# Optimization experiments

Measured on AMD Instinct MI355X. Metric: run time of the kernel, lower is better.

## Reference

```python
import math
import jax, jax.numpy as jnp
import numpy as np

NEG = -1e10


def _rope_cos_sin(T, head_dim, dtype):
    # theta_i = 10000^(-2*(i-1)/dim), i=1..dim/2  ->  j=0..dim/2-1: 10000^(-2j/dim)
    j = jnp.arange(head_dim // 2, dtype=jnp.float32)
    inv_freq = 1.0 / (10000.0 ** (2.0 * j / head_dim))
    t = jnp.arange(T, dtype=jnp.float32)
    ang = t[:, None] * inv_freq[None, :]          # [T, hd/2]
    return jnp.cos(ang).astype(dtype), jnp.sin(ang).astype(dtype)


def _apply_rope(x, cos, sin):
    # x: [B, H, T, hd]; complex multiply (cos + i sin) * (x0 + i x1)
    B, H, T, hd = x.shape
    xr = x.reshape(B, H, T, hd // 2, 2)
    x0, x1 = xr[..., 0], xr[..., 1]
    c = cos[None, None]  # [1,1,T,hd/2]
    s = sin[None, None]
    o0 = c * x0 - s * x1
    o1 = s * x0 + c * x1
    return jnp.stack([o0, o1], axis=-1).reshape(B, H, T, hd)


def setup_inputs() -> dict:
    key = jax.random.key(0)
    ks = jax.random.split(key, 9)
    B, T, C = 2, 2048, 1024
    std = 0.02
    return {
        "x": jax.random.normal(ks[0], (B, T, C), jnp.float32),
        "Wq": jax.random.normal(ks[1], (C, C), jnp.float32) * std,
        "bq": jnp.zeros((C,), jnp.float32),
        "Wk": jax.random.normal(ks[2], (C, C), jnp.float32) * std,
        "bk": jnp.zeros((C,), jnp.float32),
        "Wv": jax.random.normal(ks[3], (C, C), jnp.float32) * std,
        "bv": jnp.zeros((C,), jnp.float32),
        "Wp": jax.random.normal(ks[4], (C, C), jnp.float32) * std,
        "bp": jnp.zeros((C,), jnp.float32),
    }


def reference(x, Wq, bq, Wk, bk, Wv, bv, Wp, bp):
    B, T, C = x.shape
    H = 16
    hd = C // H

    def heads(y):  # [B,T,C] -> [B,H,T,hd]
        return y.reshape(B, T, H, hd).transpose(0, 2, 1, 3)

    q = heads(x @ Wq.T + bq)
    k = heads(x @ Wk.T + bk)
    v = heads(x @ Wv.T + bv)

    cos, sin = _rope_cos_sin(T, hd, x.dtype)
    q = _apply_rope(q, cos, sin)
    k = _apply_rope(k, cos, sin)

    att = jnp.einsum('bhqd,bhkd->bhqk', q, k) * (1.0 / math.sqrt(hd))
    causal = jnp.tril(jnp.ones((T, T), bool))
    att = jnp.where(causal[None, None], att, jnp.asarray(NEG, att.dtype))
    att = jax.nn.softmax(att, axis=-1)

    y = jnp.einsum('bhqk,bhkd->bhqd', att, v)
    y = y.transpose(0, 2, 1, 3).reshape(B, T, C)
    return y @ Wp.T + bp
```

## Files before the change

kernel.cpp:

```cpp
#include <hip/hip_runtime.h>
#include <math.h>

typedef unsigned short u16;
typedef unsigned int u32;
typedef unsigned long long u64;
typedef __attribute__((ext_vector_type(8))) short short8;
typedef __attribute__((ext_vector_type(4))) float f32x4;
typedef __attribute__((ext_vector_type(4))) u16 u16x4;
typedef __attribute__((ext_vector_type(4))) u32 u32x4;

#define AS1 __attribute__((address_space(1)))
#define AS3 __attribute__((address_space(3)))

#define QSCALE 0.18033688011112042f

__device__ __forceinline__ u16 f2bf(float f) {
  union { float f; u32 i; } u; u.f = f;
  u32 r = u.i + 0x7FFFu + ((u.i >> 16) & 1u);
  return (u16)(r >> 16);
}

__device__ __forceinline__ u32 pk_bf16(float a, float b) {
  u32 r;
  asm volatile("v_cvt_pk_bf16_f32 %0, %1, %2" : "=v"(r) : "v"(a), "v"(b));
  return r;
}

__device__ __forceinline__ void gl_lds16(const void* g, void* l) {
  __builtin_amdgcn_global_load_lds((const AS1 u32*)g, (AS3 u32*)l, 16, 0, 0);
}

#define MFMA32(a, b, c) __builtin_amdgcn_mfma_f32_16x16x32_bf16(a, b, c, 0, 0, 0)

__global__ void cvt_all(const float* __restrict__ x,
                        const float* __restrict__ Wq, const float* __restrict__ Wk,
                        const float* __restrict__ Wv, const float* __restrict__ Wp,
                        u16* __restrict__ xb,
                        u16* __restrict__ Wqb, u16* __restrict__ Wkb,
                        u16* __restrict__ Wvb, u16* __restrict__ Wpb,
                        float* __restrict__ cosT, float* __restrict__ sinT,
                        int n4x, int n4tot) {
  int i = blockIdx.x * 256 + threadIdx.x;
  if (i >= n4tot) {
    int k = i - n4tot;
    int t = k >> 5, j = k & 31;
    float inv = powf(10000.0f, -(float)j / 32.0f);
    float ang = (float)t * inv;
    cosT[k] = cosf(ang);
    sinT[k] = sinf(ang);
    return;
  }
  const float* src; u16* dst; int off;
  if (i < n4x) { src = x; dst = xb; off = i; }
  else {
    int wi = i - n4x;
    int sel = wi >> 18;
    off = wi & ((1 << 18) - 1);
    src = sel == 0 ? Wq : sel == 1 ? Wk : sel == 2 ? Wv : Wp;
    dst = sel == 0 ? Wqb : sel == 1 ? Wkb : sel == 2 ? Wvb : Wpb;
  }
  float4 v = ((const float4*)src)[off];
  u16x4 o = { f2bf(v.x), f2bf(v.y), f2bf(v.z), f2bf(v.w) };
  ((u16x4*)dst)[off] = o;
}

__global__ __launch_bounds__(256, 2) void gemm_qkv(
    const u16* __restrict__ xb,
    const u16* __restrict__ Wqb, const u16* __restrict__ Wkb, const u16* __restrict__ Wvb,
    const float* __restrict__ bq, const float* __restrict__ bk, const float* __restrict__ bv,
    const float* __restrict__ cosT, const float* __restrict__ sinT,
    u16* __restrict__ Qb, u16* __restrict__ Kb, u16* __restrict__ Vb) {
  const int K = 1024, N = 1024;
  __shared__ __attribute__((aligned(16))) u16 As[128 * 32];
  __shared__ __attribute__((aligned(16))) u16 Bs[128 * 32];
  const int tid = threadIdx.x;
  const int lane = tid & 63;
  const int hi = lane >> 4, cc = lane & 15;
  const int w = tid >> 6, wm = w >> 1, wn = w & 1;
  const int sel = blockIdx.x >> 3;
  const int row0 = blockIdx.y * 128, col0 = (blockIdx.x & 7) * 128;
  const u16* W = sel == 0 ? Wqb : sel == 1 ? Wkb : Wvb;
  const float* bias = sel == 0 ? bq : sel == 1 ? bk : bv;
  u16* Out = sel == 0 ? Qb : sel == 1 ? Kb : Vb;

  const int lr = tid >> 2;
  const int lk = (((tid & 3) ^ (lr & 3)) * 8);
  const u16* Ag0 = xb + (size_t)(row0 + lr) * K + lk;
  const u16* Ag1 = xb + (size_t)(row0 + 64 + lr) * K + lk;
  const u16* Wg0 = W + (size_t)(col0 + lr) * K + lk;
  const u16* Wg1 = W + (size_t)(col0 + 64 + lr) * K + lk;
  u16* Al0 = As + tid * 8;
  u16* Al1 = As + 2048 + tid * 8;
  u16* Bl0 = Bs + tid * 8;
  u16* Bl1 = Bs + 2048 + tid * 8;

  const int rb = (hi ^ (cc & 3)) * 8;

  f32x4 acc[4][4];
#pragma unroll
  for (int m = 0; m < 4; ++m)
#pragma unroll
    for (int n = 0; n < 4; ++n) acc[m][n] = f32x4{0.f, 0.f, 0.f, 0.f};

  for (int k0 = 0; k0 < K; k0 += 32) {
    __syncthreads();
    gl_lds16(Ag0 + k0, Al0);
    gl_lds16(Ag1 + k0, Al1);
    gl_lds16(Wg0 + k0, Bl0);
    gl_lds16(Wg1 + k0, Bl1);
    __syncthreads();
    short8 a[4], b[4];
#pragma unroll
    for (int m = 0; m < 4; ++m)
      a[m] = *(const short8*)(As + (wm * 64 + m * 16 + cc) * 32 + rb);
#pragma unroll
    for (int n = 0; n < 4; ++n)
      b[n] = *(const short8*)(Bs + (wn * 64 + n * 16 + cc) * 32 + rb);
#pragma unroll
    for (int m = 0; m < 4; ++m)
#pragma unroll
      for (int n = 0; n < 4; ++n)
        acc[m][n] = MFMA32(a[m], b[n], acc[m][n]);
  }

  if (sel < 2) {
    const float qs = (sel == 0) ? QSCALE : 1.0f;
#pragma unroll
    for (int n = 0; n < 4; ++n) {
      const int col = col0 + wn * 64 + n * 16 + cc;
      const int j = (col & 63) >> 1;
      const float bb = bias[col];
#pragma unroll
      for (int m = 0; m < 4; ++m) {
        const int rw = row0 + wm * 64 + m * 16 + hi * 4;
#pragma unroll
        for (int r = 0; r < 4; ++r) {
          const int row = rw + r;
          const int t = row & 2047;
          float v = acc[m][n][r] + bb;
          float pv = __shfl_xor(v, 1);
          float c = cosT[t * 32 + j], s = sinT[t * 32 + j];
          float oo = (cc & 1) ? (s * pv + c * v) : (c * v - s * pv);
          Out[(size_t)row * N + col] = f2bf(oo * qs);
        }
      }
    }
  } else {
#pragma unroll
    for (int n = 0; n < 4; ++n) {
      const int col = col0 + wn * 64 + n * 16 + cc;
      const float bb = bias[col];
#pragma unroll
      for (int m = 0; m < 4; ++m) {
        const int rw = row0 + wm * 64 + m * 16 + hi * 4;
#pragma unroll
        for (int r = 0; r < 4; ++r)
          Out[(size_t)(rw + r) * N + col] = f2bf(acc[m][n][r] + bb);
      }
    }
  }
}

__global__ __launch_bounds__(256, 2) void flash_mfma(
    const u16* __restrict__ Qb, const u16* __restrict__ Kb,
    const u16* __restrict__ Vb, u16* __restrict__ Yb) {
  const int T = 2048, C = 1024;
  __shared__ __attribute__((aligned(16))) u16 Ks[64 * 64];
  __shared__ __attribute__((aligned(16))) u16 Vt[64 * 64];
  __shared__ __attribute__((aligned(16))) u16 Ps[4][16 * 64];

  const int tid = threadIdx.x;
  const int lane = tid & 63;
  const int hi = lane >> 4, cc = lane & 15;
  const int hi4 = hi * 4;
  const int w = tid >> 6;
  const int qtA = blockIdx.x;
  const int qtB = 31 - qtA;
  const int bh = blockIdx.y;
  const size_t hbase = (size_t)(bh >> 4) * T * C + (size_t)(bh & 15) * 64;
  const int qA0w = qtA * 64 + w * 16;
  const int qB0w = qtB * 64 + w * 16;

  short8 qaA0, qaA1, qaB0, qaB1;
  {
    const u16* qp = Qb + hbase + (size_t)(qA0w + cc) * C + hi * 8;
    qaA0 = *(const short8*)qp;
    qaA1 = *(const short8*)(qp + 32);
    qp = Qb + hbase + (size_t)(qB0w + cc) * C + hi * 8;
    qaB0 = *(const short8*)qp;
    qaB1 = *(const short8*)(qp + 32);
  }

  f32x4 oA[4], oB[4];
#pragma unroll
  for (int nt = 0; nt < 4; ++nt) {
    oA[nt] = f32x4{0.f, 0.f, 0.f, 0.f};
    oB[nt] = f32x4{0.f, 0.f, 0.f, 0.f};
  }
  float mA = -1e30f, lA = 0.f, mB = -1e30f, lB = 0.f;

  const int krow = tid >> 2, kcol = (tid & 3) * 16;
  const int vd0 = (tid & 31) * 2, vkey0 = (tid >> 5) * 8;
  const u16* kgp = Kb + hbase + (size_t)krow * C + kcol;
  const u16* vgp = Vb + hbase + (size_t)vkey0 * C + vd0;

  short8 kr0, kr1;
  u32 vr_[8];

  auto LOADT = [&](int kt) {
    const size_t off = (size_t)(kt * 64) * C;
    kr0 = *(const short8*)(kgp + off);
    kr1 = *(const short8*)(kgp + off + 8);
#pragma unroll
    for (int j = 0; j < 8; ++j)
      vr_[j] = *(const u32*)(vgp + off + (size_t)j * C);
  };

  char* KsB = (char*)Ks;
  char* VtB = (char*)Vt;
  char* PsB = (char*)(Ps[w]);

  auto WRITET = [&]() {
    const int kb = krow * 128 + kcol * 2;
    const int ksw = (krow & 7) << 4;
    *(short8*)(KsB + (kb ^ ksw)) = kr0;
    *(short8*)(KsB + ((kb + 16) ^ ksw)) = kr1;
    u32 lo0 = (vr_[0] & 0xFFFFu) | (vr_[1] << 16);
    u32 lo1 = (vr_[2] & 0xFFFFu) | (vr_[3] << 16);
    u32 lo2 = (vr_[4] & 0xFFFFu) | (vr_[5] << 16);
    u32 lo3 = (vr_[6] & 0xFFFFu) | (vr_[7] << 16);
    u32 hh0 = (vr_[0] >> 16) | (vr_[1] & 0xFFFF0000u);
    u32 hh1 = (vr_[2] >> 16) | (vr_[3] & 0xFFFF0000u);
    u32 hh2 = (vr_[4] >> 16) | (vr_[5] & 0xFFFF0000u);
    u32 hh3 = (vr_[6] >> 16) | (vr_[7] & 0xFFFF0000u);
    const int d1 = vd0 + 1;
    u32x4 vlo = {lo0, lo1, lo2, lo3};
    u32x4 vhi = {hh0, hh1, hh2, hh3};
    *(u32x4*)(VtB + ((vd0 * 128 + vkey0 * 2) ^ ((vd0 & 7) << 4))) = vlo;
    *(u32x4*)(VtB + ((d1 * 128 + vkey0 * 2) ^ ((d1 & 7) << 4))) = vhi;
  };

  const int ksw2 = (cc & 7) << 4;
  short8 kf[4][2];

  auto CHUNK = [&](const short8& qa0, const short8& qa1, f32x4* o,
                   float& mrow, float& lsum, bool diag) {
    f32x4 s[4];
#pragma unroll
    for (int nt = 0; nt < 4; ++nt) {
      f32x4 z = f32x4{0.f, 0.f, 0.f, 0.f};
      z = MFMA32(kf[nt][0], qa0, z);
      z = MFMA32(kf[nt][1], qa1, z);
      s[nt] = z;
    }
    if (diag) {
      const int qloc = w * 16 + cc;
#pragma unroll
      for (int nt = 0; nt < 4; ++nt)
#pragma unroll
        for (int r = 0; r < 4; ++r)
          if (nt * 16 + hi4 + r > qloc) s[nt][r] = -1e30f;
    }
    float tm = s[0][0];
#pragma unroll
    for (int nt = 0; nt < 4; ++nt)
#pragma unroll
      for (int r = 0; r < 4; ++r) tm = fmaxf(tm, s[nt][r]);
    tm = fmaxf(tm, __shfl_xor(tm, 16));
    tm = fmaxf(tm, __shfl_xor(tm, 32));

    const bool need = tm > mrow + 8.0f;
    float corr = 1.0f;
    if (need) { corr = exp2f(mrow - tm); mrow = tm; }

    float psum = 0.f;
#pragma unroll
    for (int nt = 0; nt < 4; ++nt) {
      float e0 = exp2f(s[nt][0] - mrow);
      float e1 = exp2f(s[nt][1] - mrow);
      float e2 = exp2f(s[nt][2] - mrow);
      float e3 = exp2f(s[nt][3] - mrow);
      psum += (e0 + e1) + (e2 + e3);
      u32 pr[2] = { pk_bf16(e0, e1), pk_bf16(e2, e3) };
      *(u64*)(PsB + ((cc * 128 + nt * 32 + hi * 8) ^ ksw2)) = *(const u64*)pr;
    }
    psum += __shfl_xor(psum, 16);
    psum += __shfl_xor(psum, 32);
    lsum = lsum * corr + psum;
    if (__any(need)) {
#pragma unroll
      for (int nt = 0; nt < 4; ++nt) o[nt] *= corr;
    }

#pragma unroll
    for (int kc = 0; kc < 2; ++kc) {
      short8 pa = *(const short8*)(PsB + ((cc * 128 + kc * 64 + hi * 16) ^ ksw2));
#pragma unroll
      for (int nt = 0; nt < 4; ++nt) {
        short8 vb = *(const short8*)(VtB + (((nt * 16 + cc) * 128 + kc * 64 + hi * 16) ^ ksw2));
        o[nt] = MFMA32(vb, pa, o[nt]);
      }
    }
  };

  LOADT(0);
  WRITET();
  LOADT(1);
  __syncthreads();

  for (int kt = 0; kt <= qtB; ++kt) {
#pragma unroll
    for (int nt = 0; nt < 4; ++nt) {
      const int kb = (nt * 16 + cc) * 128 + hi * 16;
      kf[nt][0] = *(const short8*)(KsB + (kb ^ ksw2));
      kf[nt][1] = *(const short8*)(KsB + ((kb + 64) ^ ksw2));
    }

    CHUNK(qaB0, qaB1, oB, mB, lB, kt == qtB);
    if (kt <= qtA) CHUNK(qaA0, qaA1, oA, mA, lA, kt == qtA);

    if (kt < qtB) {
      __syncthreads();
      WRITET();
      if (kt + 1 < qtB) LOADT(kt + 2);
      __syncthreads();
    }
  }

  const float ivA = 1.0f / lA, ivB = 1.0f / lB;
#pragma unroll
  for (int nt = 0; nt < 4; ++nt) {
    u16x4 yA = { f2bf(oA[nt][0] * ivA), f2bf(oA[nt][1] * ivA),
                 f2bf(oA[nt][2] * ivA), f2bf(oA[nt][3] * ivA) };
    *(u16x4*)(Yb + hbase + (size_t)(qA0w + cc) * C + nt * 16 + hi4) = yA;
    u16x4 yB = { f2bf(oB[nt][0] * ivB), f2bf(oB[nt][1] * ivB),
                 f2bf(oB[nt][2] * ivB), f2bf(oB[nt][3] * ivB) };
    *(u16x4*)(Yb + hbase + (size_t)(qB0w + cc) * C + nt * 16 + hi4) = yB;
  }
}

__global__ __launch_bounds__(256, 2) void gemm_proj(
    const u16* __restrict__ A, const u16* __restrict__ W,
    const float* __restrict__ bias, float* __restrict__ Out) {
  const int K = 1024, N = 1024;
  __shared__ __attribute__((aligned(16))) u16 As[128 * 32];
  __shared__ __attribute__((aligned(16))) u16 Bs[64 * 32];
  const int tid = threadIdx.x;
  const int lane = tid & 63;
  const int hi = lane >> 4, cc = lane & 15;
  const int w = tid >> 6, wm = w >> 1, wn = w & 1;
  const int row0 = blockIdx.y * 128, col0 = blockIdx.x * 64;

  const int lr = tid >> 2;
  const int lk = (((tid & 3) ^ (lr & 3)) * 8);
  const u16* Ag0 = A + (size_t)(row0 + lr) * K + lk;
  const u16* Ag1 = A + (size_t)(row0 + 64 + lr) * K + lk;
  const u16* Wg0 = W + (size_t)(col0 + lr) * K + lk;
  u16* Al0 = As + tid * 8;
  u16* Al1 = As + 2048 + tid * 8;
  u16* Bl0 = Bs + tid * 8;

  const int rb = (hi ^ (cc & 3)) * 8;

  f32x4 acc[4][2];
#pragma unroll
  for (int m = 0; m < 4; ++m)
#pragma unroll
    for (int n = 0; n < 2; ++n) acc[m][n] = f32x4{0.f, 0.f, 0.f, 0.f};

  for (int k0 = 0; k0 < K; k0 += 32) {
    __syncthreads();
    gl_lds16(Ag0 + k0, Al0);
    gl_lds16(Ag1 + k0, Al1);
    gl_lds16(Wg0 + k0, Bl0);
    __syncthreads();
    short8 a[4], b[2];
#pragma unroll
    for (int m = 0; m < 4; ++m)
      a[m] = *(const short8*)(As + (wm * 64 + m * 16 + cc) * 32 + rb);
#pragma unroll
    for (int n = 0; n < 2; ++n)
      b[n] = *(const short8*)(Bs + (wn * 32 + n * 16 + cc) * 32 + rb);
#pragma unroll
    for (int m = 0; m < 4; ++m)
#pragma unroll
      for (int n = 0; n < 2; ++n)
        acc[m][n] = MFMA32(a[m], b[n], acc[m][n]);
  }

#pragma unroll
  for (int n = 0; n < 2; ++n) {
    const int col = col0 + wn * 32 + n * 16 + cc;
    const float bb = bias[col];
#pragma unroll
    for (int m = 0; m < 4; ++m) {
      const int rw = row0 + wm * 64 + m * 16 + hi * 4;
#pragma unroll
      for (int r = 0; r < 4; ++r)
        Out[(size_t)(rw + r) * N + col] = acc[m][n][r] + bb;
    }
  }
}

extern "C" void kernel_launch(void* const* d_in, const int* in_sizes, int n_in,
                              void* d_out, int out_size, void* d_ws, size_t ws_size,
                              hipStream_t stream) {
  const float* x  = (const float*)d_in[0];
  const float* Wq = (const float*)d_in[1];
  const float* bq = (const float*)d_in[2];
  const float* Wk = (const float*)d_in[3];
  const float* bk = (const float*)d_in[4];
  const float* Wv = (const float*)d_in[5];
  const float* bv = (const float*)d_in[6];
  const float* Wp = (const float*)d_in[7];
  const float* bp = (const float*)d_in[8];
  float* out = (float*)d_out;

  const int B = 2, T = 2048, C = 1024;
  const int M = B * T;
  const size_t MC = (size_t)M * C;
  const size_t CC = (size_t)C * C;

  char* p = (char*)d_ws;
  u16* xb  = (u16*)p;  p += MC * 2;
  u16* Wqb = (u16*)p;  p += CC * 2;
  u16* Wkb = (u16*)p;  p += CC * 2;
  u16* Wvb = (u16*)p;  p += CC * 2;
  u16* Wpb = (u16*)p;  p += CC * 2;
  u16* Qbb = (u16*)p;  p += MC * 2;
  u16* Kbb = (u16*)p;  p += MC * 2;
  u16* Vbb = (u16*)p;  p += MC * 2;
  float* cosT = (float*)p; p += (size_t)T * 32 * 4;
  float* sinT = (float*)p; p += (size_t)T * 32 * 4;

  const int n4x = (int)(MC / 4);
  const int n4tot = n4x + 4 * (int)(CC / 4);
  const int ntot = n4tot + T * 32;
  cvt_all<<<(ntot + 255) / 256, 256, 0, stream>>>(x, Wq, Wk, Wv, Wp,
                                                  xb, Wqb, Wkb, Wvb, Wpb,
                                                  cosT, sinT, n4x, n4tot);

  dim3 gq(24, M / 128);
  gemm_qkv<<<gq, 256, 0, stream>>>(xb, Wqb, Wkb, Wvb, bq, bk, bv, cosT, sinT, Qbb, Kbb, Vbb);

  dim3 fg(16, B * 16);
  flash_mfma<<<fg, 256, 0, stream>>>(Qbb, Kbb, Vbb, xb);

  dim3 gp(C / 64, M / 128);
  gemm_proj<<<gp, 256, 0, stream>>>(xb, Wpb, bp, out);
}
```

Baseline: 128.1 us.

## Double GEMM K-tile to 64 and interleave two query chunks in flash attention

Both GEMM kernels move from a K-step of 32 to 64, using a wider 8-way XOR swizzle in LDS. This halves the number of barrier pairs per K loop and issues more MFMAs between syncs, at the cost of twice the shared memory per block. The flash attention loop now computes QK^T for both query chunks before either softmax, and gives each chunk its own P buffer. It also loads the V fragments once from LDS and reuses them for both PV products, which cuts redundant LDS reads and exposes more independent MFMA work, but raises register pressure.

Result: faster. 124.2 us (-3.1%).

```diff
diff --git a/kernel.cpp b/kernel.cpp
--- a/kernel.cpp
+++ b/kernel.cpp
@@ -71,8 +71,8 @@
     const float* __restrict__ cosT, const float* __restrict__ sinT,
     u16* __restrict__ Qb, u16* __restrict__ Kb, u16* __restrict__ Vb) {
   const int K = 1024, N = 1024;
-  __shared__ __attribute__((aligned(16))) u16 As[128 * 32];
-  __shared__ __attribute__((aligned(16))) u16 Bs[128 * 32];
+  __shared__ __attribute__((aligned(16))) u16 As[128 * 64];
+  __shared__ __attribute__((aligned(16))) u16 Bs[128 * 64];
   const int tid = threadIdx.x;
   const int lane = tid & 63;
   const int hi = lane >> 4, cc = lane & 15;
@@ -83,18 +83,10 @@
   const float* bias = sel == 0 ? bq : sel == 1 ? bk : bv;
   u16* Out = sel == 0 ? Qb : sel == 1 ? Kb : Vb;
 
-  const int lr = tid >> 2;
-  const int lk = (((tid & 3) ^ (lr & 3)) * 8);
-  const u16* Ag0 = xb + (size_t)(row0 + lr) * K + lk;
-  const u16* Ag1 = xb + (size_t)(row0 + 64 + lr) * K + lk;
-  const u16* Wg0 = W + (size_t)(col0 + lr) * K + lk;
-  const u16* Wg1 = W + (size_t)(col0 + 64 + lr) * K + lk;
-  u16* Al0 = As + tid * 8;
-  u16* Al1 = As + 2048 + tid * 8;
-  u16* Bl0 = Bs + tid * 8;
-  u16* Bl1 = Bs + 2048 + tid * 8;
-
-  const int rb = (hi ^ (cc & 3)) * 8;
+  const int lr = tid >> 3;
+  const int lkb = (((tid & 7) ^ (lr & 7)) * 8);
+  const u16* Ag = xb + (size_t)(row0 + lr) * K + lkb;
+  const u16* Wg = W + (size_t)(col0 + lr) * K + lkb;
 
   f32x4 acc[4][4];
 #pragma unroll
@@ -102,25 +94,33 @@
 #pragma unroll
     for (int n = 0; n < 4; ++n) acc[m][n] = f32x4{0.f, 0.f, 0.f, 0.f};
 
-  for (int k0 = 0; k0 < K; k0 += 32) {
+  for (int k0 = 0; k0 < K; k0 += 64) {
     __syncthreads();
-    gl_lds16(Ag0 + k0, Al0);
-    gl_lds16(Ag1 + k0, Al1);
-    gl_lds16(Wg0 + k0, Bl0);
-    gl_lds16(Wg1 + k0, Bl1);
+#pragma unroll
+    for (int j = 0; j < 4; ++j) {
+      gl_lds16(Ag + (size_t)j * 32 * K + k0, As + j * 2048 + tid * 8);
+      gl_lds16(Wg + (size_t)j * 32 * K + k0, Bs + j * 2048 + tid * 8);
+    }
     __syncthreads();
-    short8 a[4], b[4];
-#pragma unroll
-    for (int m = 0; m < 4; ++m)
-      a[m] = *(const short8*)(As + (wm * 64 + m * 16 + cc) * 32 + rb);
-#pragma unroll
-    for (int n = 0; n < 4; ++n)
-      b[n] = *(const short8*)(Bs + (wn * 64 + n * 16 + cc) * 32 + rb);
-#pragma unroll
-    for (int m = 0; m < 4; ++m)
+    short8 a[2][4], b[2][4];
+#pragma unroll
+    for (int kk = 0; kk < 2; ++kk) {
+#pragma unroll
+      for (int m = 0; m < 4; ++m)
+        a[kk][m] = *(const short8*)(As + (wm * 64 + m * 16 + cc) * 64 +
+                                    (((kk * 4 + hi) ^ (cc & 7)) * 8));
 #pragma unroll
       for (int n = 0; n < 4; ++n)
-        acc[m][n] = MFMA32(a[m], b[n], acc[m][n]);
+        b[kk][n] = *(const short8*)(Bs + (wn * 64 + n * 16 + cc) * 64 +
+                                    (((kk * 4 + hi) ^ (cc & 7)) * 8));
+    }
+#pragma unroll
+    for (int kk = 0; kk < 2; ++kk)
+#pragma unroll
+      for (int m = 0; m < 4; ++m)
+#pragma unroll
+        for (int n = 0; n < 4; ++n)
+          acc[m][n] = MFMA32(a[kk][m], b[kk][n], acc[m][n]);
   }
 
   if (sel < 2) {
@@ -167,7 +167,7 @@
   const int T = 2048, C = 1024;
   __shared__ __attribute__((aligned(16))) u16 Ks[64 * 64];
   __shared__ __attribute__((aligned(16))) u16 Vt[64 * 64];
-  __shared__ __attribute__((aligned(16))) u16 Ps[4][16 * 64];
+  __shared__ __attribute__((aligned(16))) u16 Ps[4][2][16 * 64];
 
   const int tid = threadIdx.x;
   const int lane = tid & 63;
@@ -218,7 +218,8 @@
 
   char* KsB = (char*)Ks;
   char* VtB = (char*)Vt;
-  char* PsB = (char*)(Ps[w]);
+  char* PsA_ = (char*)(Ps[w][0]);
+  char* PsB_ = (char*)(Ps[w][1]);
 
   auto WRITET = [&]() {
     const int kb = krow * 128 + kcol * 2;
@@ -241,11 +242,9 @@
   };
 
   const int ksw2 = (cc & 7) << 4;
-  short8 kf[4][2];
-
-  auto CHUNK = [&](const short8& qa0, const short8& qa1, f32x4* o,
-                   float& mrow, float& lsum, bool diag) {
-    f32x4 s[4];
+
+  auto QKT = [&](short8 (&kf)[4][2], const short8& qa0, const short8& qa1,
+                 f32x4 (&s)[4]) {
 #pragma unroll
     for (int nt = 0; nt < 4; ++nt) {
       f32x4 z = f32x4{0.f, 0.f, 0.f, 0.f};
@@ -253,14 +252,9 @@
       z = MFMA32(kf[nt][1], qa1, z);
       s[nt] = z;
     }
-    if (diag) {
-      const int qloc = w * 16 + cc;
-#pragma unroll
-      for (int nt = 0; nt < 4; ++nt)
-#pragma unroll
-        for (int r = 0; r < 4; ++r)
-          if (nt * 16 + hi4 + r > qloc) s[nt][r] = -1e30f;
-    }
+  };
+
+  auto SM = [&](f32x4 (&s)[4], float& mrow, float& lsum, f32x4* o, char* PsX) {
     float tm = s[0][0];
 #pragma unroll
     for (int nt = 0; nt < 4; ++nt)
@@ -268,11 +262,9 @@
       for (int r = 0; r < 4; ++r) tm = fmaxf(tm, s[nt][r]);
     tm = fmaxf(tm, __shfl_xor(tm, 16));
     tm = fmaxf(tm, __shfl_xor(tm, 32));
-
     const bool need = tm > mrow + 8.0f;
     float corr = 1.0f;
     if (need) { corr = exp2f(mrow - tm); mrow = tm; }
-
     float psum = 0.f;
 #pragma unroll
     for (int nt = 0; nt < 4; ++nt) {
@@ -282,7 +274,7 @@
       float e3 = exp2f(s[nt][3] - mrow);
       psum += (e0 + e1) + (e2 + e3);
       u32 pr[2] = { pk_bf16(e0, e1), pk_bf16(e2, e3) };
-      *(u64*)(PsB + ((cc * 128 + nt * 32 + hi * 8) ^ ksw2)) = *(const u64*)pr;
+      *(u64*)(PsX + ((cc * 128 + nt * 32 + hi * 8) ^ ksw2)) = *(const u64*)pr;
     }
     psum += __shfl_xor(psum, 16);
     psum += __shfl_xor(psum, 32);
@@ -291,16 +283,15 @@
 #pragma unroll
       for (int nt = 0; nt < 4; ++nt) o[nt] *= corr;
     }
-
-#pragma unroll
-    for (int kc = 0; kc < 2; ++kc) {
-      short8 pa = *(const short8*)(PsB + ((cc * 128 + kc * 64 + hi * 16) ^ ksw2));
-#pragma unroll
-      for (int nt = 0; nt < 4; ++nt) {
-        short8 vb = *(const short8*)(VtB + (((nt * 16 + cc) * 128 + kc * 64 + hi * 16) ^ ksw2));
-        o[nt] = MFMA32(vb, pa, o[nt]);
-      }
-    }
+  };
+
+  auto MASK = [&](f32x4 (&s)[4]) {
+    const int qloc = w * 16 + cc;
+#pragma unroll
+    for (int nt = 0; nt < 4; ++nt)
+#pragma unroll
+      for (int r = 0; r < 4; ++r)
+        if (nt * 16 + hi4 + r > qloc) s[nt][r] = -1e30f;
   };
 
   LOADT(0);
@@ -309,6 +300,7 @@
   __syncthreads();
 
   for (int kt = 0; kt <= qtB; ++kt) {
+    short8 kf[4][2];
 #pragma unroll
     for (int nt = 0; nt < 4; ++nt) {
       const int kb = (nt * 16 + cc) * 128 + hi * 16;
@@ -316,8 +308,39 @@
       kf[nt][1] = *(const short8*)(KsB + ((kb + 64) ^ ksw2));
     }
 
-    CHUNK(qaB0, qaB1, oB, mB, lB, kt == qtB);
-    if (kt <= qtA) CHUNK(qaA0, qaA1, oA, mA, lA, kt == qtA);
+    const bool actA = (kt <= qtA);
+    f32x4 sB[4], sA[4];
+    QKT(kf, qaB0, qaB1, sB);
+    if (actA) QKT(kf, qaA0, qaA1, sA);
+    if (kt == qtB) MASK(sB);
+    if (actA && kt == qtA) MASK(sA);
+
+    SM(sB, mB, lB, oB, PsB_);
+    if (actA) SM(sA, mA, lA, oA, PsA_);
+
+    short8 vf[2][4];
+#pragma unroll
+    for (int kc = 0; kc < 2; ++kc)
+#pragma unroll
+      for (int nt = 0; nt < 4; ++nt)
+        vf[kc][nt] = *(const short8*)(VtB + (((nt * 16 + cc) * 128 + kc * 64 + hi * 16) ^ ksw2));
+
+#pragma unroll
+    for (int kc = 0; kc < 2; ++kc) {
+      short8 pa = *(const short8*)(PsB_ + ((cc * 128 + kc * 64 + hi * 16) ^ ksw2));
+#pragma unroll
+      for (int nt = 0; nt < 4; ++nt)
+        oB[nt] = MFMA32(vf[kc][nt], pa, oB[nt]);
+    }
+    if (actA) {
+#pragma unroll
+      for (int kc = 0; kc < 2; ++kc) {
+        short8 pa = *(const short8*)(PsA_ + ((cc * 128 + kc * 64 + hi * 16) ^ ksw2));
+#pragma unroll
+        for (int nt = 0; nt < 4; ++nt)
+          oA[nt] = MFMA32(vf[kc][nt], pa, oA[nt]);
+      }
+    }
 
     if (kt < qtB) {
       __syncthreads();
@@ -343,24 +366,18 @@
     const u16* __restrict__ A, const u16* __restrict__ W,
     const float* __restrict__ bias, float* __restrict__ Out) {
   const int K = 1024, N = 1024;
-  __shared__ __attribute__((aligned(16))) u16 As[128 * 32];
-  __shared__ __attribute__((aligned(16))) u16 Bs[64 * 32];
+  __shared__ __attribute__((aligned(16))) u16 As[128 * 64];
+  __shared__ __attribute__((aligned(16))) u16 Bs[64 * 64];
   const int tid = threadIdx.x;
   const int lane = tid & 63;
   const int hi = lane >> 4, cc = lane & 15;
   const int w = tid >> 6, wm = w >> 1, wn = w & 1;
   const int row0 = blockIdx.y * 128, col0 = blockIdx.x * 64;
 
-  const int lr = tid >> 2;
-  const int lk = (((tid & 3) ^ (lr & 3)) * 8);
-  const u16* Ag0 = A + (size_t)(row0 + lr) * K + lk;
-  const u16* Ag1 = A + (size_t)(row0 + 64 + lr) * K + lk;
-  const u16* Wg0 = W + (size_t)(col0 + lr) * K + lk;
-  u16* Al0 = As + tid * 8;
-  u16* Al1 = As + 2048 + tid * 8;
-  u16* Bl0 = Bs + tid * 8;
-
-  const int rb = (hi ^ (cc & 3)) * 8;
+  const int lr = tid >> 3;
+  const int lkb = (((tid & 7) ^ (lr & 7)) * 8);
+  const u16* Ag = A + (size_t)(row0 + lr) * K + lkb;
+  const u16* Wg = W + (size_t)(col0 + lr) * K + lkb;
 
   f32x4 acc[4][2];
 #pragma unroll
@@ -368,24 +385,34 @@
 #pragma unroll
     for (int n = 0; n < 2; ++n) acc[m][n] = f32x4{0.f, 0.f, 0.f, 0.f};
 
-  for (int k0 = 0; k0 < K; k0 += 32) {
+  for (int k0 = 0; k0 < K; k0 += 64) {
     __syncthreads();
-    gl_lds16(Ag0 + k0, Al0);
-    gl_lds16(Ag1 + k0, Al1);
-    gl_lds16(Wg0 + k0, Bl0);
+#pragma unroll
+    for (int j = 0; j < 4; ++j)
+      gl_lds16(Ag + (size_t)j * 32 * K + k0, As + j * 2048 + tid * 8);
+#pragma unroll
+    for (int j = 0; j < 2; ++j)
+      gl_lds16(Wg + (size_t)j * 32 * K + k0, Bs + j * 2048 + tid * 8);
     __syncthreads();
-    short8 a[4], b[2];
-#pragma unroll
-    for (int m = 0; m < 4; ++m)
-      a[m] = *(const short8*)(As + (wm * 64 + m * 16 + cc) * 32 + rb);
-#pragma unroll
-    for (int n = 0; n < 2; ++n)
-      b[n] = *(const short8*)(Bs + (wn * 32 + n * 16 + cc) * 32 + rb);
-#pragma unroll
-    for (int m = 0; m < 4; ++m)
+    short8 a[2][4], b[2][2];
+#pragma unroll
+    for (int kk = 0; kk < 2; ++kk) {
+#pragma unroll
+      for (int m = 0; m < 4; ++m)
+        a[kk][m] = *(const short8*)(As + (wm * 64 + m * 16 + cc) * 64 +
+                                    (((kk * 4 + hi) ^ (cc & 7)) * 8));
 #pragma unroll
       for (int n = 0; n < 2; ++n)
-        acc[m][n] = MFMA32(a[m], b[n], acc[m][n]);
+        b[kk][n] = *(const short8*)(Bs + (wn * 32 + n * 16 + cc) * 64 +
+                                    (((kk * 4 + hi) ^ (cc & 7)) * 8));
+    }
+#pragma unroll
+    for (int kk = 0; kk < 2; ++kk)
+#pragma unroll
+      for (int m = 0; m < 4; ++m)
+#pragma unroll
+        for (int n = 0; n < 2; ++n)
+          acc[m][n] = MFMA32(a[kk][m], b[kk][n], acc[m][n]);
   }
 
 #pragma unroll
```
